# Performance work log

Hardware: AMD Instinct MI355X
Metric: run time of the kernel (lower is better)

## Reference

```python
import jax, jax.numpy as jnp
import numpy as np

L_KERNELS = 15
STRIDE = 1
DIMS = [60, 72, 86, 86, 71, 59]  # indim=4*15, then *1.2,*1.2, mid, /1.2,/1.2 per __init__


def setup_inputs() -> dict:
    key = jax.random.key(0)
    ks = jax.random.split(key, 13)
    B, C, L, K = 16, 4, 1000, 64
    inp = {"x": jax.random.normal(ks[0], (B, C, L), jnp.float32)}
    for i in range(5):
        di, do = DIMS[i], DIMS[i + 1]
        inp[f"w{i}"] = jax.random.normal(ks[1 + 2 * i], (K, di, do), jnp.float32) * (1.0 / np.sqrt(di))
        inp[f"b{i}"] = jax.random.normal(ks[2 + 2 * i], (K, do), jnp.float32) * 0.01
    inp["head_w"] = jax.random.normal(ks[11], (DIMS[5], 1), jnp.float32) * (1.0 / np.sqrt(DIMS[5]))
    inp["head_b"] = jax.random.normal(ks[12], (1,), jnp.float32) * 0.01
    return inp


def reference(x, w0, b0, w1, b1, w2, b2, w3, b3, w4, b4, head_w, head_b):
    B, C, L = x.shape
    l, s = L_KERNELS, STRIDE
    n_out = (L - l) // s + 1
    # unfold: (B, C, n_out, l) via gather of sliding windows
    idx = jnp.arange(n_out)[:, None] * s + jnp.arange(l)[None, :]
    xw = x[:, :, idx]
    # transpose(-2,-3) then flatten(start_dim=3): (B, n_out, C*l)
    xw = jnp.transpose(xw, (0, 2, 1, 3)).reshape(B, n_out, C * l)
    # per-kernel FC stack: broadcast-mul+sum in torch == grouped matmul here
    h = jax.nn.gelu(jnp.einsum('bld,kde->bkle', xw, w0) + b0[None, :, None, :], approximate=False)
    for w, b in ((w1, b1), (w2, b2), (w3, b3), (w4, b4)):
        h = jax.nn.gelu(jnp.einsum('bkld,kde->bkle', h, w) + b[None, :, None, :], approximate=False)
    out = (h @ head_w + head_b).squeeze(-1)  # (B, K, n_out)
    return out
```

## Files before the change

kernel.cpp:

```cpp
#include <hip/hip_runtime.h>

typedef _Float16 f16;
typedef __attribute__((ext_vector_type(8))) _Float16 f16x8;
typedef __attribute__((ext_vector_type(2))) __fp16 hf16x2;
typedef __attribute__((ext_vector_type(4))) float f32x4;

constexpr int C_ = 4, L_ = 1000, K_ = 64, NOUT = 986, NPOS = 16 * 986;
constexpr int TPB  = 256;
constexpr int MTB  = 128;
constexpr int NBLK = (NPOS + MTB - 1) / MTB;
constexpr int AST  = 104;
constexpr int ACT_EL  = MTB * AST;
constexpr size_t SMEM_BYTES = (size_t)ACT_EL * 2 + 480 * 4 + 64 * 4;

constexpr size_t WOFF[5]  = {0, 638976, 1277952, 1916928, 2555904};
constexpr int    WROWS[5] = {80, 96, 96, 80, 64};
constexpr int    DIv[5]   = {60, 72, 86, 86, 71};
constexpr int    DOv[5]   = {72, 86, 86, 71, 59};

__device__ __forceinline__ float gelu_f(float x) {
    float x2 = x * x;
    float z  = x * __builtin_fmaf(0.0356774081f, x2, 0.7978845608f);
    float e  = __expf(-2.0f * z);
    return x * __builtin_amdgcn_rcpf(e + 1.0f);
}

template<int MT>
__device__ __forceinline__ void pre_a(const f16* __restrict__ wsrc, f16x8 (&ap)[6],
                                      int li, int q) {
#pragma unroll
    for (int mt = 0; mt < MT; mt++)
        ap[mt] = *(const f16x8*)(wsrc + (mt * 16 + li) * AST + q * 8);
}

template<int KSTEPS, int MT>
__device__ __forceinline__ void layer_mm_p(const f16* __restrict__ actw,
                                           const f16* __restrict__ wsrc,
                                           const f16x8 (&ap)[6],
                                           f32x4 (&acc)[MT][2], int li, int q) {
#pragma unroll
    for (int mt = 0; mt < MT; mt++)
#pragma unroll
        for (int nt = 0; nt < 2; nt++) acc[mt][nt] = f32x4{0.f, 0.f, 0.f, 0.f};
#pragma unroll
    for (int ks = 0; ks < KSTEPS; ks++) {
        const int koff = ks * 32 + q * 8;
        f16x8 a[MT], b[2];
#pragma unroll
        for (int mt = 0; mt < MT; mt++)
            a[mt] = (ks == 0) ? ap[mt]
                              : *(const f16x8*)(wsrc + (mt * 16 + li) * AST + koff);
#pragma unroll
        for (int nt = 0; nt < 2; nt++)
            b[nt] = *(const f16x8*)(actw + (nt * 16 + li) * AST + koff);
#pragma unroll
        for (int mt = 0; mt < MT; mt++)
#pragma unroll
            for (int nt = 0; nt < 2; nt++)
                acc[mt][nt] = __builtin_amdgcn_mfma_f32_16x16x32_f16(a[mt], b[nt], acc[mt][nt], 0, 0, 0);
    }
}

template<int MT>
__device__ __forceinline__ void epilogue(f32x4 (&acc)[MT][2], f16* __restrict__ actw,
                                         const float* __restrict__ bl, int li, int q) {
#pragma unroll
    for (int mt = 0; mt < MT; mt++) {
        const int eb = mt * 16 + q * 4;
        f32x4 bb = *(const f32x4*)(bl + eb);
#pragma unroll
        for (int nt = 0; nt < 2; nt++) {
            union { hf16x2 h[2]; unsigned long long u; } pk;
            pk.h[0] = __builtin_amdgcn_cvt_pkrtz(gelu_f(acc[mt][nt][0] + bb[0]),
                                                 gelu_f(acc[mt][nt][1] + bb[1]));
            pk.h[1] = __builtin_amdgcn_cvt_pkrtz(gelu_f(acc[mt][nt][2] + bb[2]),
                                                 gelu_f(acc[mt][nt][3] + bb[3]));
            f16* dst = actw + (nt * 16 + li) * AST + eb;
            *(unsigned long long*)dst = pk.u;
        }
    }
}

template<int L>
__device__ __forceinline__ void prep_one(const float* __restrict__ wsrc0, f16* __restrict__ ws,
                                         f16* __restrict__ wl, int k, int tid) {
    constexpr int DI = DIv[L], DO = DOv[L], RW = WROWS[L];
    const float* wsrc = wsrc0 + (size_t)k * DI * DO;
    constexpr int TOT = DI * DO;
    constexpr int NIT = (TOT + 255) / 256;
    float v[NIT];
#pragma unroll
    for (int it = 0; it < NIT; it++) {
        int i = tid + it * 256;
        v[it] = (i < TOT) ? wsrc[i] : 0.f;
    }
#pragma unroll
    for (int it = 0; it < NIT; it++) {
        int i = tid + it * 256;
        if (i < TOT) {
            int d = i / DO, e = i - d * DO;
            wl[d * 87 + e] = (f16)v[it];
        }
    }
    __syncthreads();
    f16* dst = ws + WOFF[L] + (size_t)k * 96 * AST;
    constexpr int CH = RW * 13;
    constexpr int NIT2 = (CH + 255) / 256;
#pragma unroll
    for (int it = 0; it < NIT2; it++) {
        int c = tid + it * 256;
        if (c < CH) {
            int e = c / 13, db = (c - e * 13) * 8;
            f16x8 vv;
#pragma unroll
            for (int j = 0; j < 8; j++) {
                int d = db + j;
                vv[j] = (e < DO && d < DI) ? wl[d * 87 + e] : (f16)0.f;
            }
            *(f16x8*)(dst + (size_t)c * 8) = vv;
        }
    }
}

__global__ __launch_bounds__(256) void prep_weights(
    const float* __restrict__ w0, const float* __restrict__ w1, const float* __restrict__ w2,
    const float* __restrict__ w3, const float* __restrict__ w4, f16* __restrict__ ws) {
    __shared__ f16 wl[86 * 87];
    const int k = blockIdx.x, tid = threadIdx.x;
    switch (blockIdx.y) {
        case 0: prep_one<0>(w0, ws, wl, k, tid); break;
        case 1: prep_one<1>(w1, ws, wl, k, tid); break;
        case 2: prep_one<2>(w2, ws, wl, k, tid); break;
        case 3: prep_one<3>(w3, ws, wl, k, tid); break;
        default: prep_one<4>(w4, ws, wl, k, tid); break;
    }
}

__global__ __launch_bounds__(TPB, 4) void mlp_main(
    const float* __restrict__ x,
    const float* __restrict__ b0, const float* __restrict__ b1, const float* __restrict__ b2,
    const float* __restrict__ b3, const float* __restrict__ b4,
    const float* __restrict__ hw, const float* __restrict__ hb,
    const f16* __restrict__ ws, float* __restrict__ out) {
    extern __shared__ char smemraw[];
    f16*   act   = (f16*)smemraw;
    float* biasl = (float*)(act + ACT_EL);
    float* headl = biasl + 480;

    const int tid = threadIdx.x, k = blockIdx.x, mblk = blockIdx.y;
    const int wv = tid >> 6, lane = tid & 63, li = lane & 15, q = lane >> 4;
    const int base = mblk * MTB;
    f16* actw = act + (wv * 32) * AST;
    const f16* wk = ws + (size_t)k * 96 * AST;

    f16x8 ap[6];
    pre_a<5>(wk + WOFF[0], ap, li, q);

    for (int i = tid; i < 480; i += TPB) {
        int l = i / 96, e = i - l * 96;
        const float* bg = (l == 0) ? b0 : (l == 1) ? b1 : (l == 2) ? b2 : (l == 3) ? b3 : b4;
        int DO = (l == 0) ? 72 : (l == 1) ? 86 : (l == 2) ? 86 : (l == 3) ? 71 : 59;
        biasl[i] = (e < DO) ? bg[k * DO + e] : 0.f;
    }
    if (tid < 64) headl[tid] = (tid < 59) ? hw[tid] : 0.f;

    {
        const int b0i = base / NOUT;
        const int thr = (b0i + 1) * NOUT;
        for (int i = tid; i < 64 * MTB; i += TPB) {
            int d = i >> 7, r = i & (MTB - 1);
            int p = base + r; if (p > NPOS - 1) p = NPOS - 1;
            int b = (p >= thr) ? b0i + 1 : b0i;
            int pos = p - b * NOUT;
            float v = 0.f;
            if (d < 60) { int c = d / 15, j = d - c * 15; v = x[(size_t)(b * C_ + c) * L_ + pos + j]; }
            act[r * AST + d] = (f16)v;
        }
    }
    for (int i = tid; i < MTB * 2; i += TPB) {
        int r = i >> 1, cc = (i & 1) << 3;
        *(f16x8*)(act + r * AST + 80 + cc) = f16x8{0,0,0,0,0,0,0,0};
    }
    const float hb0 = hb[0];
    __syncthreads();

    f32x4 acc[6][2];
    f32x4 (&acc5)[5][2] = reinterpret_cast<f32x4 (&)[5][2]>(acc);

    layer_mm_p<2, 5>(actw, wk + WOFF[0], ap, acc5, li, q);
    pre_a<6>(wk + WOFF[1], ap, li, q);
    epilogue<5>(acc5, actw, biasl + 0 * 96, li, q);
    layer_mm_p<3, 6>(actw, wk + WOFF[1], ap, acc, li, q);
    pre_a<6>(wk + WOFF[2], ap, li, q);
    epilogue<6>(acc, actw, biasl + 1 * 96, li, q);
    layer_mm_p<3, 6>(actw, wk + WOFF[2], ap, acc, li, q);
    pre_a<5>(wk + WOFF[3], ap, li, q);
    epilogue<6>(acc, actw, biasl + 2 * 96, li, q);
    layer_mm_p<3, 5>(actw, wk + WOFF[3], ap, acc5, li, q);
    pre_a<4>(wk + WOFF[4], ap, li, q);
    epilogue<5>(acc5, actw, biasl + 3 * 96, li, q);

    f32x4 acc4[4][2];
    layer_mm_p<3, 4>(actw, wk + WOFF[4], ap, acc4, li, q);
    float sum[2] = {0.f, 0.f};
#pragma unroll
    for (int mt = 0; mt < 4; mt++) {
        const int eb = mt * 16 + q * 4;
        f32x4 bb = *(const f32x4*)(biasl + 4 * 96 + eb);
        f32x4 hh = *(const f32x4*)(headl + eb);
#pragma unroll
        for (int nt = 0; nt < 2; nt++) {
#pragma unroll
            for (int r = 0; r < 4; r++)
                sum[nt] += gelu_f(acc4[mt][nt][r] + bb[r]) * hh[r];
        }
    }
#pragma unroll
    for (int nt = 0; nt < 2; nt++) {
        float s = sum[nt];
        s += __shfl_xor(s, 16);
        s += __shfl_xor(s, 32);
        s += hb0;
        if (lane < 16) {
            int p = base + wv * 32 + nt * 16 + lane;
            if (p < NPOS) {
                int b = p / NOUT, pos = p - b * NOUT;
                out[((size_t)(b * K_ + k)) * NOUT + pos] = s;
            }
        }
    }
}

extern "C" void kernel_launch(void* const* d_in, const int* in_sizes, int n_in,
                              void* d_out, int out_size, void* d_ws, size_t ws_size,
                              hipStream_t stream) {
    const float* x  = (const float*)d_in[0];
    const float* w0 = (const float*)d_in[1];  const float* b0 = (const float*)d_in[2];
    const float* w1 = (const float*)d_in[3];  const float* b1 = (const float*)d_in[4];
    const float* w2 = (const float*)d_in[5];  const float* b2 = (const float*)d_in[6];
    const float* w3 = (const float*)d_in[7];  const float* b3 = (const float*)d_in[8];
    const float* w4 = (const float*)d_in[9];  const float* b4 = (const float*)d_in[10];
    const float* hw = (const float*)d_in[11]; const float* hb = (const float*)d_in[12];
    float* out = (float*)d_out;
    f16* ws = (f16*)d_ws;

    (void)hipFuncSetAttribute((const void*)mlp_main,
                              hipFuncAttributeMaxDynamicSharedMemorySize, (int)SMEM_BYTES);

    prep_weights<<<dim3(K_, 5), 256, 0, stream>>>(w0, w1, w2, w3, w4, ws);
    mlp_main<<<dim3(K_, NBLK), TPB, SMEM_BYTES, stream>>>(x, b0, b1, b2, b3, b4, hw, hb, ws, out);
}
```

Before: 292.8 us.

## Prefetch full weight panels into registers and double-buffer activation loads

Each layer's whole weight panel (all k-steps) is now loaded from global memory into registers before the previous layer's epilogue, not just the first k-step. The activation B-fragments are double-buffered across k-steps so LDS reads overlap the MFMAs. GELU now uses exp2 with the constants pre-scaled, removing a multiply. Occupancy is lowered from 4 to 3 blocks per SM to make room for the larger register footprint, which risks less latency hiding.

```diff
diff --git a/kernel.cpp b/kernel.cpp
--- a/kernel.cpp
+++ b/kernel.cpp
@@ -20,44 +20,52 @@
 
 __device__ __forceinline__ float gelu_f(float x) {
     float x2 = x * x;
-    float z  = x * __builtin_fmaf(0.0356774081f, x2, 0.7978845608f);
-    float e  = __expf(-2.0f * z);
+    float ei = x * __builtin_fmaf(-0.1029433270f, x2, -2.3022082020f);
+    float e  = __builtin_amdgcn_exp2f(ei);
     return x * __builtin_amdgcn_rcpf(e + 1.0f);
 }
 
-template<int MT>
-__device__ __forceinline__ void pre_a(const f16* __restrict__ wsrc, f16x8 (&ap)[6],
-                                      int li, int q) {
+template<int KSTEPS, int MT>
+__device__ __forceinline__ void pre_panel(const f16* __restrict__ wsrc, f16x8 (&ap)[18],
+                                          int li, int q) {
+#pragma unroll
+    for (int ks = 0; ks < KSTEPS; ks++)
+#pragma unroll
+        for (int mt = 0; mt < MT; mt++)
+            ap[ks * MT + mt] = *(const f16x8*)(wsrc + (mt * 16 + li) * AST + ks * 32 + q * 8);
+}
+
+template<int KSTEPS, int MT>
+__device__ __forceinline__ void layer_mm_r(const f16* __restrict__ actw,
+                                           const f16x8 (&ap)[18],
+                                           f32x4 (&acc)[MT][2], int li, int q) {
 #pragma unroll
     for (int mt = 0; mt < MT; mt++)
-        ap[mt] = *(const f16x8*)(wsrc + (mt * 16 + li) * AST + q * 8);
-}
-
-template<int KSTEPS, int MT>
-__device__ __forceinline__ void layer_mm_p(const f16* __restrict__ actw,
-                                           const f16* __restrict__ wsrc,
-                                           const f16x8 (&ap)[6],
-                                           f32x4 (&acc)[MT][2], int li, int q) {
-#pragma unroll
-    for (int mt = 0; mt < MT; mt++)
 #pragma unroll
         for (int nt = 0; nt < 2; nt++) acc[mt][nt] = f32x4{0.f, 0.f, 0.f, 0.f};
+    f16x8 b[2];
+#pragma unroll
+    for (int nt = 0; nt < 2; nt++)
+        b[nt] = *(const f16x8*)(actw + (nt * 16 + li) * AST + q * 8);
 #pragma unroll
     for (int ks = 0; ks < KSTEPS; ks++) {
-        const int koff = ks * 32 + q * 8;
-        f16x8 a[MT], b[2];
+        f16x8 bn[2];
+        if (ks + 1 < KSTEPS) {
+            const int koff = (ks + 1) * 32 + q * 8;
+#pragma unroll
+            for (int nt = 0; nt < 2; nt++)
+                bn[nt] = *(const f16x8*)(actw + (nt * 16 + li) * AST + koff);
+        }
 #pragma unroll
         for (int mt = 0; mt < MT; mt++)
-            a[mt] = (ks == 0) ? ap[mt]
-                              : *(const f16x8*)(wsrc + (mt * 16 + li) * AST + koff);
-#pragma unroll
-        for (int nt = 0; nt < 2; nt++)
-            b[nt] = *(const f16x8*)(actw + (nt * 16 + li) * AST + koff);
-#pragma unroll
-        for (int mt = 0; mt < MT; mt++)
 #pragma unroll
             for (int nt = 0; nt < 2; nt++)
-                acc[mt][nt] = __builtin_amdgcn_mfma_f32_16x16x32_f16(a[mt], b[nt], acc[mt][nt], 0, 0, 0);
+                acc[mt][nt] = __builtin_amdgcn_mfma_f32_16x16x32_f16(ap[ks * MT + mt], b[nt],
+                                                                     acc[mt][nt], 0, 0, 0);
+        if (ks + 1 < KSTEPS) {
+#pragma unroll
+            for (int nt = 0; nt < 2; nt++) b[nt] = bn[nt];
+        }
     }
 }
 
@@ -136,7 +144,7 @@
     }
 }
 
-__global__ __launch_bounds__(TPB, 4) void mlp_main(
+__global__ __launch_bounds__(TPB, 3) void mlp_main(
     const float* __restrict__ x,
     const float* __restrict__ b0, const float* __restrict__ b1, const float* __restrict__ b2,
     const float* __restrict__ b3, const float* __restrict__ b4,
@@ -153,8 +161,8 @@
     f16* actw = act + (wv * 32) * AST;
     const f16* wk = ws + (size_t)k * 96 * AST;
 
-    f16x8 ap[6];
-    pre_a<5>(wk + WOFF[0], ap, li, q);
+    f16x8 ap[18];
+    pre_panel<2, 5>(wk + WOFF[0], ap, li, q);
 
     for (int i = tid; i < 480; i += TPB) {
         int l = i / 96, e = i - l * 96;
@@ -187,21 +195,21 @@
     f32x4 acc[6][2];
     f32x4 (&acc5)[5][2] = reinterpret_cast<f32x4 (&)[5][2]>(acc);
 
-    layer_mm_p<2, 5>(actw, wk + WOFF[0], ap, acc5, li, q);
-    pre_a<6>(wk + WOFF[1], ap, li, q);
+    layer_mm_r<2, 5>(actw, ap, acc5, li, q);
+    pre_panel<3, 6>(wk + WOFF[1], ap, li, q);
     epilogue<5>(acc5, actw, biasl + 0 * 96, li, q);
-    layer_mm_p<3, 6>(actw, wk + WOFF[1], ap, acc, li, q);
-    pre_a<6>(wk + WOFF[2], ap, li, q);
+    layer_mm_r<3, 6>(actw, ap, acc, li, q);
+    pre_panel<3, 6>(wk + WOFF[2], ap, li, q);
     epilogue<6>(acc, actw, biasl + 1 * 96, li, q);
-    layer_mm_p<3, 6>(actw, wk + WOFF[2], ap, acc, li, q);
-    pre_a<5>(wk + WOFF[3], ap, li, q);
+    layer_mm_r<3, 6>(actw, ap, acc, li, q);
+    pre_panel<3, 5>(wk + WOFF[3], ap, li, q);
     epilogue<6>(acc, actw, biasl + 2 * 96, li, q);
-    layer_mm_p<3, 5>(actw, wk + WOFF[3], ap, acc5, li, q);
-    pre_a<4>(wk + WOFF[4], ap, li, q);
+    layer_mm_r<3, 5>(actw, ap, acc5, li, q);
+    pre_panel<3, 4>(wk + WOFF[4], ap, li, q);
     epilogue<5>(acc5, actw, biasl + 3 * 96, li, q);
 
     f32x4 acc4[4][2];
-    layer_mm_p<3, 4>(actw, wk + WOFF[4], ap, acc4, li, q);
+    layer_mm_r<3, 4>(actw, ap, acc4, li, q);
     float sum[2] = {0.f, 0.f};
 #pragma unroll
     for (int mt = 0; mt < 4; mt++) {
```

New measurement: 296.5 us. No clear change (+1.3%).

## Precompute fp16 input windows once and stream them into LDS via global_load_lds

Applied to the files above, without the earlier changes.

Adds a prep pass that builds each 128-row fp16 unfolded input tile once in workspace, so each of the 64 per-kernel blocks copies it straight into LDS with global_load_lds instead of redoing the gather and convert. Bias is folded into the accumulator initialisation, and GELU now uses a direct exp2 with pre-scaled constants. This removes redundant gather work repeated 64 times, at the cost of extra workspace and a larger prep launch. It falls back to the old path if the workspace is too small.

```diff
diff --git a/kernel.cpp b/kernel.cpp
--- a/kernel.cpp
+++ b/kernel.cpp
@@ -17,11 +17,14 @@
 constexpr int    WROWS[5] = {80, 96, 96, 80, 64};
 constexpr int    DIv[5]   = {60, 72, 86, 86, 71};
 constexpr int    DOv[5]   = {72, 86, 86, 71, 59};
+constexpr size_t WTOT    = WOFF[4] + (size_t)K_ * 96 * AST;
+constexpr size_t ACT_WS  = WTOT;
+constexpr size_t WS_NEED = (WTOT + (size_t)NBLK * ACT_EL) * 2;
 
 __device__ __forceinline__ float gelu_f(float x) {
     float x2 = x * x;
-    float z  = x * __builtin_fmaf(0.0356774081f, x2, 0.7978845608f);
-    float e  = __expf(-2.0f * z);
+    float ei = x * __builtin_fmaf(-0.1029433270f, x2, -2.3022082020f);
+    float e  = __builtin_amdgcn_exp2f(ei);
     return x * __builtin_amdgcn_rcpf(e + 1.0f);
 }
 
@@ -37,11 +40,14 @@
 __device__ __forceinline__ void layer_mm_p(const f16* __restrict__ actw,
                                            const f16* __restrict__ wsrc,
                                            const f16x8 (&ap)[6],
-                                           f32x4 (&acc)[MT][2], int li, int q) {
-#pragma unroll
-    for (int mt = 0; mt < MT; mt++)
-#pragma unroll
-        for (int nt = 0; nt < 2; nt++) acc[mt][nt] = f32x4{0.f, 0.f, 0.f, 0.f};
+                                           f32x4 (&acc)[MT][2],
+                                           const float* __restrict__ bl, int li, int q) {
+#pragma unroll
+    for (int mt = 0; mt < MT; mt++) {
+        f32x4 bb = *(const f32x4*)(bl + mt * 16 + q * 4);
+#pragma unroll
+        for (int nt = 0; nt < 2; nt++) acc[mt][nt] = bb;
+    }
 #pragma unroll
     for (int ks = 0; ks < KSTEPS; ks++) {
         const int koff = ks * 32 + q * 8;
@@ -63,18 +69,17 @@
 
 template<int MT>
 __device__ __forceinline__ void epilogue(f32x4 (&acc)[MT][2], f16* __restrict__ actw,
-                                         const float* __restrict__ bl, int li, int q) {
+                                         int li, int q) {
 #pragma unroll
     for (int mt = 0; mt < MT; mt++) {
         const int eb = mt * 16 + q * 4;
-        f32x4 bb = *(const f32x4*)(bl + eb);
 #pragma unroll
         for (int nt = 0; nt < 2; nt++) {
             union { hf16x2 h[2]; unsigned long long u; } pk;
-            pk.h[0] = __builtin_amdgcn_cvt_pkrtz(gelu_f(acc[mt][nt][0] + bb[0]),
-                                                 gelu_f(acc[mt][nt][1] + bb[1]));
-            pk.h[1] = __builtin_amdgcn_cvt_pkrtz(gelu_f(acc[mt][nt][2] + bb[2]),
-                                                 gelu_f(acc[mt][nt][3] + bb[3]));
+            pk.h[0] = __builtin_amdgcn_cvt_pkrtz(gelu_f(acc[mt][nt][0]),
+                                                 gelu_f(acc[mt][nt][1]));
+            pk.h[1] = __builtin_amdgcn_cvt_pkrtz(gelu_f(acc[mt][nt][2]),
+                                                 gelu_f(acc[mt][nt][3]));
             f16* dst = actw + (nt * 16 + li) * AST + eb;
             *(unsigned long long*)dst = pk.u;
         }
@@ -122,11 +127,29 @@
     }
 }
 
+__device__ __forceinline__ void prep_act(const float* __restrict__ x, f16* __restrict__ dst0,
+                                         int m, int tid) {
+    f16* dst = dst0 + (size_t)m * ACT_EL;
+    const int base = m * MTB;
+    for (int i = tid; i < ACT_EL; i += 256) {
+        int r = i / AST, c = i - r * AST;
+        int p = base + r; if (p > NPOS - 1) p = NPOS - 1;
+        int b = p / NOUT, pos = p - b * NOUT;
+        float v = 0.f;
+        if (c < 60) { int ch = c / 15, j = c - ch * 15; v = x[(size_t)(b * C_ + ch) * L_ + pos + j]; }
+        dst[i] = (f16)v;
+    }
+}
+
 __global__ __launch_bounds__(256) void prep_weights(
     const float* __restrict__ w0, const float* __restrict__ w1, const float* __restrict__ w2,
-    const float* __restrict__ w3, const float* __restrict__ w4, f16* __restrict__ ws) {
+    const float* __restrict__ w3, const float* __restrict__ w4,
+    const float* __restrict__ x, f16* __restrict__ ws) {
     __shared__ f16 wl[86 * 87];
-    const int k = blockIdx.x, tid = threadIdx.x;
+    const int tid = threadIdx.x;
+    if (blockIdx.y == 5) { prep_act(x, ws + ACT_WS, blockIdx.x, tid); return; }
+    const int k = blockIdx.x;
+    if (k >= K_) return;
     switch (blockIdx.y) {
         case 0: prep_one<0>(w0, ws, wl, k, tid); break;
         case 1: prep_one<1>(w1, ws, wl, k, tid); break;
@@ -136,6 +159,7 @@
     }
 }
 
+template<bool PRE>
 __global__ __launch_bounds__(TPB, 4) void mlp_main(
     const float* __restrict__ x,
     const float* __restrict__ b0, const float* __restrict__ b1, const float* __restrict__ b2,
@@ -164,7 +188,14 @@
     }
     if (tid < 64) headl[tid] = (tid < 59) ? hw[tid] : 0.f;
 
-    {
+    if constexpr (PRE) {
+        const f16* src = ws + ACT_WS + (size_t)mblk * ACT_EL;
+        for (int c = wv; c < 26; c += 4) {
+            __builtin_amdgcn_global_load_lds(
+                (const __attribute__((address_space(1))) void*)(src + c * 512 + lane * 8),
+                (__attribute__((address_space(3))) void*)(act + c * 512), 16, 0, 0);
+        }
+    } else {
         const int b0i = base / NOUT;
         const int thr = (b0i + 1) * NOUT;
         for (int i = tid; i < 64 * MTB; i += TPB) {
@@ -176,10 +207,10 @@
             if (d < 60) { int c = d / 15, j = d - c * 15; v = x[(size_t)(b * C_ + c) * L_ + pos + j]; }
             act[r * AST + d] = (f16)v;
         }
-    }
-    for (int i = tid; i < MTB * 2; i += TPB) {
-        int r = i >> 1, cc = (i & 1) << 3;
-        *(f16x8*)(act + r * AST + 80 + cc) = f16x8{0,0,0,0,0,0,0,0};
+        for (int i = tid; i < MTB * 2; i += TPB) {
+            int r = i >> 1, cc = (i & 1) << 3;
+            *(f16x8*)(act + r * AST + 80 + cc) = f16x8{0,0,0,0,0,0,0,0};
+        }
     }
     const float hb0 = hb[0];
     __syncthreads();
@@ -187,32 +218,31 @@
     f32x4 acc[6][2];
     f32x4 (&acc5)[5][2] = reinterpret_cast<f32x4 (&)[5][2]>(acc);
 
-    layer_mm_p<2, 5>(actw, wk + WOFF[0], ap, acc5, li, q);
+    layer_mm_p<2, 5>(actw, wk + WOFF[0], ap, acc5, biasl + 0 * 96, li, q);
     pre_a<6>(wk + WOFF[1], ap, li, q);
-    epilogue<5>(acc5, actw, biasl + 0 * 96, li, q);
-    layer_mm_p<3, 6>(actw, wk + WOFF[1], ap, acc, li, q);
+    epilogue<5>(acc5, actw, li, q);
+    layer_mm_p<3, 6>(actw, wk + WOFF[1], ap, acc, biasl + 1 * 96, li, q);
     pre_a<6>(wk + WOFF[2], ap, li, q);
-    epilogue<6>(acc, actw, biasl + 1 * 96, li, q);
-    layer_mm_p<3, 6>(actw, wk + WOFF[2], ap, acc, li, q);
+    epilogue<6>(acc, actw, li, q);
+    layer_mm_p<3, 6>(actw, wk + WOFF[2], ap, acc, biasl + 2 * 96, li, q);
     pre_a<5>(wk + WOFF[3], ap, li, q);
-    epilogue<6>(acc, actw, biasl + 2 * 96, li, q);
-    layer_mm_p<3, 5>(actw, wk + WOFF[3], ap, acc5, li, q);
+    epilogue<6>(acc, actw, li, q);
+    layer_mm_p<3, 5>(actw, wk + WOFF[3], ap, acc5, biasl + 3 * 96, li, q);
     pre_a<4>(wk + WOFF[4], ap, li, q);
-    epilogue<5>(acc5, actw, biasl + 3 * 96, li, q);
+    epilogue<5>(acc5, actw, li, q);
 
     f32x4 acc4[4][2];
-    layer_mm_p<3, 4>(actw, wk + WOFF[4], ap, acc4, li, q);
+    layer_mm_p<3, 4>(actw, wk + WOFF[4], ap, acc4, biasl + 4 * 96, li, q);
     float sum[2] = {0.f, 0.f};
 #pragma unroll
     for (int mt = 0; mt < 4; mt++) {
         const int eb = mt * 16 + q * 4;
-        f32x4 bb = *(const f32x4*)(biasl + 4 * 96 + eb);
         f32x4 hh = *(const f32x4*)(headl + eb);
 #pragma unroll
         for (int nt = 0; nt < 2; nt++) {
 #pragma unroll
             for (int r = 0; r < 4; r++)
-                sum[nt] += gelu_f(acc4[mt][nt][r] + bb[r]) * hh[r];
+                sum[nt] += gelu_f(acc4[mt][nt][r]) * hh[r];
         }
     }
 #pragma unroll
@@ -244,9 +274,19 @@
     float* out = (float*)d_out;
     f16* ws = (f16*)d_ws;
 
-    (void)hipFuncSetAttribute((const void*)mlp_main,
-                              hipFuncAttributeMaxDynamicSharedMemorySize, (int)SMEM_BYTES);
-
-    prep_weights<<<dim3(K_, 5), 256, 0, stream>>>(w0, w1, w2, w3, w4, ws);
-    mlp_main<<<dim3(K_, NBLK), TPB, SMEM_BYTES, stream>>>(x, b0, b1, b2, b3, b4, hw, hb, ws, out);
-}
+    const bool pre = (ws_size >= WS_NEED);
+
+    if (pre) {
+        (void)hipFuncSetAttribute((const void*)mlp_main<true>,
+                                  hipFuncAttributeMaxDynamicSharedMemorySize, (int)SMEM_BYTES);
+        prep_weights<<<dim3(NBLK, 6), 256, 0, stream>>>(w0, w1, w2, w3, w4, x, ws);
+        mlp_main<true><<<dim3(K_, NBLK), TPB, SMEM_BYTES, stream>>>(
+            x, b0, b1, b2, b3, b4, hw, hb, ws, out);
+    } else {
+        (void)hipFuncSetAttribute((const void*)mlp_main<false>,
+                                  hipFuncAttributeMaxDynamicSharedMemorySize, (int)SMEM_BYTES);
+        prep_weights<<<dim3(K_, 5), 256, 0, stream>>>(w0, w1, w2, w3, w4, x, ws);
+        mlp_main<false><<<dim3(K_, NBLK), TPB, SMEM_BYTES, stream>>>(
+            x, b0, b1, b2, b3, b4, hw, hb, ws, out);
+    }
+}
```

New measurement: 253.7 us. 13.3% less time.
